# Performance work log

Measured on AMD Instinct MI355X. Metric: run time of the kernel, lower is better.

Reference implementation:

```python
import jax, jax.numpy as jnp
import numpy as np
from jax import lax

PEAK_THRESH = 0.1
PAF_SCORE_THRESH = 0.05
PAF_COUNT_THRESH = 0.8
P = 30   # max peaks kept per joint (vectorized stand-in for data-dependent nonzero())
S = 10   # samples along each limb line (torch.linspace steps=10)

# standard COCO person skeleton: 19 limbs over 17 keypoints
SKELETON = np.array([
    [15, 13], [13, 11], [16, 14], [14, 12], [11, 12], [5, 11], [6, 12], [5, 6],
    [5, 7], [6, 8], [7, 9], [8, 10], [1, 2], [0, 1], [0, 2], [1, 3], [2, 4],
    [3, 5], [4, 6],
])  # (L=19, 2)


def setup_inputs() -> dict:
    key = jax.random.key(0)
    k1, k2 = jax.random.split(key)
    heat_pred = jax.random.uniform(k1, (32, 17, 160, 160), dtype=jnp.float32)
    paf_pred = jax.random.normal(k2, (32, 38, 160, 160), dtype=jnp.float32)
    return {"heat_pred": heat_pred, "paf_pred": paf_pred}


def _forward(heat_pred, paf_pred):
    B, K, H, W = heat_pred.shape
    L = SKELETON.shape[0]

    # ---- 3x3 peak NMS (max_pool2d k=3, s=1, p=1) ----
    pooled = lax.reduce_window(heat_pred, -jnp.inf, lax.max,
                               (1, 1, 3, 3), (1, 1, 1, 1), 'SAME')
    is_peak = (heat_pred == pooled) & (heat_pred > PEAK_THRESH)

    # ---- dense subpixel (1D Newton) offsets ----
    r = jnp.roll(heat_pred, -1, -1); l = jnp.roll(heat_pred, 1, -1)
    d = jnp.roll(heat_pred, -1, -2); u = jnp.roll(heat_pred, 1, -2)
    dx_raw = 0.5 * (r - l); dy_raw = 0.5 * (d - u)
    dxx = r + l - 2.0 * heat_pred; dyy = d + u - 2.0 * heat_pred
    safe_dxx = jnp.where(jnp.abs(dxx) > 1e-6, -dxx, 1.0)
    safe_dyy = jnp.where(jnp.abs(dyy) > 1e-6, -dyy, 1.0)
    dx = jnp.where(jnp.abs(dxx) > 1e-6, dx_raw / safe_dxx, dx_raw)
    dy = jnp.where(jnp.abs(dyy) > 1e-6, dy_raw / safe_dyy, dy_raw)
    xi = jnp.arange(W); yi = jnp.arange(H)
    interior = (((yi > 0) & (yi < H - 1))[:, None]
                & ((xi > 0) & (xi < W - 1))[None, :])
    dx = jnp.where(interior, dx, 0.0)
    dy = jnp.where(interior, dy, 0.0)

    # ---- top-P peaks per (batch, joint) ----
    NEG = jnp.float32(-1e9)
    flat = jnp.where(is_peak, heat_pred, NEG).reshape(B, K, H * W)
    scores, idx = lax.top_k(flat, P)                    # (B, K, P)
    valid = scores > PEAK_THRESH
    py = (idx // W).astype(jnp.float32)
    px = (idx % W).astype(jnp.float32)
    dxp = jnp.take_along_axis(dx.reshape(B, K, H * W), idx, axis=2)
    dyp = jnp.take_along_axis(dy.reshape(B, K, H * W), idx, axis=2)
    px = jnp.where(valid, px + dxp, 0.0)
    py = jnp.where(valid, py + dyp, 0.0)
    sc = jnp.where(valid, scores, 0.0)
    peaks = jnp.stack([px, py, sc], axis=-1)            # (B, K, P, 3)

    # ---- PAF line-integral connection scores for all candidate pairs ----
    a = SKELETON[:, 0]; b = SKELETON[:, 1]
    ax, ay, sa, va = px[:, a], py[:, a], sc[:, a], valid[:, a]   # (B, L, P)
    bx, by, sb, vb = px[:, b], py[:, b], sc[:, b], valid[:, b]
    dxl = bx[:, :, None, :] - ax[:, :, :, None]          # (B, L, P, P)
    dyl = by[:, :, None, :] - ay[:, :, :, None]
    norm = jnp.sqrt(dxl * dxl + dyl * dyl) + 1e-8
    vx = dxl / norm; vy = dyl / norm
    t = jnp.linspace(0.0, 1.0, S, dtype=jnp.float32)     # (S,)
    xs = ax[:, :, :, None, None] + t * dxl[..., None]    # (B, L, P, P, S)
    ys = ay[:, :, :, None, None] + t * dyl[..., None]
    ix = jnp.clip(jnp.round(xs), 0, W - 1).astype(jnp.int32)
    iy = jnp.clip(jnp.round(ys), 0, H - 1).astype(jnp.int32)
    lin = (iy * W + ix).reshape(B, L, P * P * S)
    paf = paf_pred.reshape(B, L, 2, H * W)
    vals_x = jnp.take_along_axis(paf[:, :, 0], lin, axis=2).reshape(B, L, P, P, S)
    vals_y = jnp.take_along_axis(paf[:, :, 1], lin, axis=2).reshape(B, L, P, P, S)
    vecs = vals_x * vx[..., None] + vals_y * vy[..., None]
    mean_score = vecs.mean(-1)                            # (B, L, P, P)
    valid_ratio = (vecs > PAF_SCORE_THRESH).astype(jnp.float32).mean(-1)
    pair_valid = va[:, :, :, None] & vb[:, :, None, :]
    cond = (mean_score > 0.0) & (valid_ratio > PAF_COUNT_THRESH) & pair_valid
    conn = jnp.where(cond,
                     mean_score + 0.5 * (sa[:, :, :, None] + sb[:, :, None, :]),
                     0.0)                                 # (B, L, P, P)
    return peaks, conn


def reference(heat_pred, paf_pred):
    return _forward(heat_pred, paf_pred)
```

## Files before the change

### kernel.cpp

```cpp
#include <hip/hip_runtime.h>
#include <cstdint>
#include <cstddef>
#include <cfloat>

static constexpr int BATCH = 32;
static constexpr int KJ    = 17;
static constexpr int LL    = 19;
static constexpr int HH    = 160;
static constexpr int WW    = 160;
static constexpr int PPK   = 30;
static constexpr int SS    = 10;
static constexpr int HW    = HH * WW;
static constexpr int CGW   = WW / 4;
static constexpr int CAP   = 4096;
static constexpr int HICAP = 512;
static constexpr int NPAIR = PPK * PPK;
static constexpr int HALFP = NPAIR / 2;
#define HITHR 0.98f

static constexpr int QROWS = 40;
static constexpr int QCNT  = QROWS * WW;
static constexpr int QF4   = QCNT / 4;

__constant__ int d_ska[LL] = {15,13,16,14,11,5,6,5,5,6,7,8,1,0,0,1,2,3,4};
__constant__ int d_skb[LL] = {13,11,14,12,12,11,12,6,7,8,9,10,2,1,2,3,4,5,6};
__constant__ float d_ts[SS] = {
    0.0f,
    (float)(1.0/9.0), (float)(2.0/9.0), (float)(3.0/9.0),
    (float)(4.0/9.0), (float)(5.0/9.0), (float)(6.0/9.0),
    (float)(7.0/9.0), (float)(8.0/9.0),
    1.0f
};

__device__ __forceinline__ float max3f(float a, float b, float c) {
    return fmaxf(fmaxf(a, b), c);
}
__device__ __forceinline__ unsigned long long umax64(unsigned long long a, unsigned long long b) {
    return a > b ? a : b;
}
__device__ __forceinline__ void async_copy16(const float4* gsrc_lane, float4* lds_wave_base) {
    __builtin_amdgcn_global_load_lds(
        (const __attribute__((address_space(1))) void*)gsrc_lane,
        (__attribute__((address_space(3))) void*)lds_wave_base,
        16, 0, 0);
}

__global__ __launch_bounds__(512, 4) void peaks_kernel(const float* __restrict__ heat,
                                                       float* __restrict__ out)
{
    const int ch = blockIdx.x;
    const float* hp = heat + (size_t)ch * HW;

    __shared__ unsigned long long keys[CAP];
    __shared__ unsigned long long hikeys[HICAP];
    __shared__ unsigned long long sel8[8 * PPK];
    __shared__ unsigned long long sel[PPK];
    __shared__ int cnt;
    __shared__ int hcnt;

    const int tid  = threadIdx.x;
    const int lane = tid & 63;
    const int wave = tid >> 6;
    const unsigned long long ltmask = ((unsigned long long)1 << lane) - 1ull;

    if (tid == 0) { cnt = 0; hcnt = 0; }
    __syncthreads();

    for (int c = tid; c < HW / 4; c += 512) {
        int y  = c / CGW;
        int cg = c - y * CGW;
        int x0 = cg * 4;
        int yu = (y > 0) ? y - 1 : 0;
        int yd = (y < HH - 1) ? y + 1 : HH - 1;

        const float* rc = hp + y  * WW + x0;
        const float* ru = hp + yu * WW + x0;
        const float* rd = hp + yd * WW + x0;

        float4 vc = *(const float4*)rc;
        float4 vu = *(const float4*)ru;
        float4 vd = *(const float4*)rd;

        int offL = (x0 > 0) ? -1 : 0;
        int offR = (x0 + 4 < WW) ? 4 : 3;
        float lc  = rc[offL], lu  = ru[offL], ld  = rd[offL];
        float rcx = rc[offR], rux = ru[offR], rdx = rd[offR];

        float mu0 = max3f(lu, vu.x, vu.y), mu1 = max3f(vu.x, vu.y, vu.z);
        float mu2 = max3f(vu.y, vu.z, vu.w), mu3 = max3f(vu.z, vu.w, rux);
        float mc0 = max3f(lc, vc.x, vc.y), mc1 = max3f(vc.x, vc.y, vc.z);
        float mc2 = max3f(vc.y, vc.z, vc.w), mc3 = max3f(vc.z, vc.w, rcx);
        float md0 = max3f(ld, vd.x, vd.y), md1 = max3f(vd.x, vd.y, vd.z);
        float md2 = max3f(vd.y, vd.z, vd.w), md3 = max3f(vd.z, vd.w, rdx);

        float nm0 = max3f(mu0, mc0, md0);
        float nm1 = max3f(mu1, mc1, md1);
        float nm2 = max3f(mu2, mc2, md2);
        float nm3 = max3f(mu3, mc3, md3);

        bool pk0 = (vc.x == nm0) && (vc.x > 0.1f);
        bool pk1 = (vc.y == nm1) && (vc.y > 0.1f);
        bool pk2 = (vc.z == nm2) && (vc.z > 0.1f);
        bool pk3 = (vc.w == nm3) && (vc.w > 0.1f);

        int idx0 = y * WW + x0;
        unsigned long long key0 = ((unsigned long long)__float_as_uint(vc.x) << 32) | (unsigned long long)(0xFFFFFFFFu - (unsigned)(idx0 + 0));
        unsigned long long key1 = ((unsigned long long)__float_as_uint(vc.y) << 32) | (unsigned long long)(0xFFFFFFFFu - (unsigned)(idx0 + 1));
        unsigned long long key2 = ((unsigned long long)__float_as_uint(vc.z) << 32) | (unsigned long long)(0xFFFFFFFFu - (unsigned)(idx0 + 2));
        unsigned long long key3 = ((unsigned long long)__float_as_uint(vc.w) << 32) | (unsigned long long)(0xFFFFFFFFu - (unsigned)(idx0 + 3));

        {
            unsigned long long b0 = __ballot(pk0);
            unsigned long long b1 = __ballot(pk1);
            unsigned long long b2 = __ballot(pk2);
            unsigned long long b3 = __ballot(pk3);
            int c0 = __popcll(b0), c1 = __popcll(b1), c2 = __popcll(b2), c3 = __popcll(b3);
            int tot = c0 + c1 + c2 + c3;
            int base = 0;
            if (lane == 0 && tot > 0) base = atomicAdd(&cnt, tot);
            base = __shfl(base, 0);
            if (pk0) { int s = base + __popcll(b0 & ltmask); if (s < CAP) keys[s] = key0; }
            if (pk1) { int s = base + c0 + __popcll(b1 & ltmask); if (s < CAP) keys[s] = key1; }
            if (pk2) { int s = base + c0 + c1 + __popcll(b2 & ltmask); if (s < CAP) keys[s] = key2; }
            if (pk3) { int s = base + c0 + c1 + c2 + __popcll(b3 & ltmask); if (s < CAP) keys[s] = key3; }
        }
        {
            bool h0 = pk0 && (vc.x > HITHR);
            bool h1 = pk1 && (vc.y > HITHR);
            bool h2 = pk2 && (vc.z > HITHR);
            bool h3 = pk3 && (vc.w > HITHR);
            unsigned long long b0 = __ballot(h0);
            unsigned long long b1 = __ballot(h1);
            unsigned long long b2 = __ballot(h2);
            unsigned long long b3 = __ballot(h3);
            int c0 = __popcll(b0), c1 = __popcll(b1), c2 = __popcll(b2), c3 = __popcll(b3);
            int tot = c0 + c1 + c2 + c3;
            int base = 0;
            if (lane == 0 && tot > 0) base = atomicAdd(&hcnt, tot);
            base = __shfl(base, 0);
            if (h0) { int s = base + __popcll(b0 & ltmask); if (s < HICAP) hikeys[s] = key0; }
            if (h1) { int s = base + c0 + __popcll(b1 & ltmask); if (s < HICAP) hikeys[s] = key1; }
            if (h2) { int s = base + c0 + c1 + __popcll(b2 & ltmask); if (s < HICAP) hikeys[s] = key2; }
            if (h3) { int s = base + c0 + c1 + c2 + __popcll(b3 & ltmask); if (s < HICAP) hikeys[s] = key3; }
        }
    }
    __syncthreads();

    const int hn = hcnt;
    if (hn >= PPK && hn <= HICAP) {
        if (wave == 0) {
            unsigned long long k[8];
            #pragma unroll
            for (int i = 0; i < 8; ++i) {
                int p = lane + i * 64;
                k[i] = (p < hn) ? hikeys[p] : 0ull;
            }
            for (int r = 0; r < PPK; ++r) {
                unsigned long long best = 0ull;
                #pragma unroll
                for (int i = 0; i < 8; ++i) best = umax64(best, k[i]);
                #pragma unroll
                for (int off = 1; off < 64; off <<= 1)
                    best = umax64(best, (unsigned long long)__shfl_xor((long long)best, off));
                if (best != 0ull) {
                    #pragma unroll
                    for (int i = 0; i < 8; ++i)
                        if (k[i] == best) k[i] = 0ull;
                }
                if (lane == 0) sel[r] = best;
            }
        }
    } else {
        const int n = (cnt < CAP) ? cnt : CAP;
        unsigned long long k[8];
        {
            int base0 = wave * 512 + lane;
            #pragma unroll
            for (int i = 0; i < 8; ++i) {
                int p = base0 + i * 64;
                k[i] = (p < n) ? keys[p] : 0ull;
            }
        }
        for (int r = 0; r < PPK; ++r) {
            unsigned long long best = 0ull;
            #pragma unroll
            for (int i = 0; i < 8; ++i) best = umax64(best, k[i]);
            #pragma unroll
            for (int off = 1; off < 64; off <<= 1)
                best = umax64(best, (unsigned long long)__shfl_xor((long long)best, off));
            if (best != 0ull) {
                #pragma unroll
                for (int i = 0; i < 8; ++i)
                    if (k[i] == best) k[i] = 0ull;
            }
            if (lane == 0) sel8[wave * PPK + r] = best;
        }
        __syncthreads();
        if (wave == 0) {
            unsigned long long m[4];
            #pragma unroll
            for (int i = 0; i < 4; ++i) {
                int p = lane + i * 64;
                m[i] = (p < 8 * PPK) ? sel8[p] : 0ull;
            }
            for (int r = 0; r < PPK; ++r) {
                unsigned long long best = umax64(umax64(m[0], m[1]), umax64(m[2], m[3]));
                #pragma unroll
                for (int off = 1; off < 64; off <<= 1)
                    best = umax64(best, (unsigned long long)__shfl_xor((long long)best, off));
                if (best != 0ull) {
                    #pragma unroll
                    for (int i = 0; i < 4; ++i)
                        if (m[i] == best) m[i] = 0ull;
                }
                if (lane == 0) sel[r] = best;
            }
        }
    }
    __syncthreads();

    if (tid < PPK) {
        unsigned long long g = sel[tid];
        float px = 0.0f, py = 0.0f, sc = 0.0f;
        if (g != 0ull) {
            float v = __uint_as_float((unsigned int)(g >> 32));
            int idx = (int)(0xFFFFFFFFu - (unsigned int)(g & 0xFFFFFFFFull));
            int y = idx / WW;
            int x = idx - y * WW;
            float dx = 0.0f, dy = 0.0f;
            if (x > 0 && x < WW - 1 && y > 0 && y < HH - 1) {
                float r_ = hp[y * WW + x + 1];
                float l_ = hp[y * WW + x - 1];
                float dn = hp[(y + 1) * WW + x];
                float up = hp[(y - 1) * WW + x];
                float dx_raw = 0.5f * (r_ - l_);
                float dy_raw = 0.5f * (dn - up);
                float dxx = __fsub_rn(__fadd_rn(r_, l_), 2.0f * v);
                float dyy = __fsub_rn(__fadd_rn(dn, up), 2.0f * v);
                dx = (fabsf(dxx) > 1e-6f) ? (dx_raw / (-dxx)) : dx_raw;
                dy = (fabsf(dyy) > 1e-6f) ? (dy_raw / (-dyy)) : dy_raw;
            }
            px = __fadd_rn((float)x, dx);
            py = __fadd_rn((float)y, dy);
            sc = v;
        }
        float* o = out + ((size_t)ch * PPK + tid) * 3;
        o[0] = px;
        o[1] = py;
        o[2] = sc;
    }
}

__global__ __launch_bounds__(512, 4) void conn_kernel(const float* __restrict__ paf,
                                                      const float* __restrict__ peaks,
                                                      float* __restrict__ conn)
{
    const int bl = blockIdx.x;
    const int b  = bl / LL;
    const int l  = bl - b * LL;

    __shared__ float buf[2][QCNT];
    __shared__ float As[PPK * 3];
    __shared__ float Bs[PPK * 3];

    const int tid  = threadIdx.x;
    const int lane = tid & 63;
    const int wave = tid >> 6;
    {
        const float* pa = peaks + (((size_t)b * KJ) + d_ska[l]) * (PPK * 3);
        const float* pb = peaks + (((size_t)b * KJ) + d_skb[l]) * (PPK * 3);
        if (tid < PPK * 3)            As[tid] = pa[tid];
        else if (tid < 2 * PPK * 3)   Bs[tid - PPK * 3] = pb[tid - PPK * 3];
    }

    const float*  src  = paf + (((size_t)b * (2 * LL)) + 2 * l) * HW;
    const float4* src4 = (const float4*)src;

    {
        float4* b4 = (float4*)buf[0];
        #pragma unroll
        for (int c = 0; c < 3; ++c)
            async_copy16(src4 + c * 512 + tid, b4 + c * 512 + wave * 64);
        if (wave == 0)
            async_copy16(src4 + 1536 + lane, b4 + 1536);
    }
    __syncthreads();

    const bool active = (tid < HALFP);
    const int p0 = active ? tid : (NPAIR - 1);
    const int p1 = active ? (tid + HALFP) : (NPAIR - 1);

    int   lin[2][SS];
    float accv[2][SS];
    float vxp[2], vyp[2], sap[2], sbp[2];

    #pragma unroll
    for (int q = 0; q < 2; ++q) {
        int p = (q == 0) ? p0 : p1;
        int i = p / PPK;
        int j = p - i * PPK;
        float ax = As[i * 3 + 0], ay = As[i * 3 + 1], sa = As[i * 3 + 2];
        float bx = Bs[j * 3 + 0], by = Bs[j * 3 + 1], sb = Bs[j * 3 + 2];
        float dxl = __fsub_rn(bx, ax);
        float dyl = __fsub_rn(by, ay);
        float nsq = __fadd_rn(__fmul_rn(dxl, dxl), __fmul_rn(dyl, dyl));
        float nrm = __fadd_rn(sqrtf(nsq), 1e-8f);
        vxp[q] = dxl / nrm;
        vyp[q] = dyl / nrm;
        sap[q] = sa;
        sbp[q] = sb;
        #pragma unroll
        for (int s = 0; s < SS; ++s) {
            float t  = d_ts[s];
            float xs = __fadd_rn(ax, __fmul_rn(t, dxl));
            float ys = __fadd_rn(ay, __fmul_rn(t, dyl));
            float rx = rintf(xs);
            float ry = rintf(ys);
            rx = fminf(fmaxf(rx, 0.0f), (float)(WW - 1));
            ry = fminf(fmaxf(ry, 0.0f), (float)(HH - 1));
            lin[q][s] = (int)ry * WW + (int)rx;
        }
    }

    for (int qq = 0; qq < 8; ++qq) {
        const int cur = qq & 1;
        if (qq < 7) {
            const int nq = qq + 1;
            const float4* s4 = (const float4*)(src + (size_t)(nq >> 2) * HW + (nq & 3) * QCNT);
            float4* b4 = (float4*)buf[1 - cur];
            #pragma unroll
            for (int c = 0; c < 3; ++c)
                async_copy16(s4 + c * 512 + tid, b4 + c * 512 + wave * 64);
            if (wave == 0)
                async_copy16(s4 + 1536 + lane, b4 + 1536);
        }
        const int comp = qq >> 2;
        const int lo   = (qq & 3) * QCNT;
        #pragma unroll
        for (int q = 0; q < 2; ++q) {
            #pragma unroll
            for (int s = 0; s < SS; ++s) {
                int lrel = lin[q][s] - lo;
                if ((unsigned)lrel < (unsigned)QCNT) {
                    float v = buf[cur][lrel];
                    if (comp == 0) accv[q][s] = __fmul_rn(v, vxp[q]);
                    else           accv[q][s] = __fadd_rn(accv[q][s], __fmul_rn(v, vyp[q]));
                }
            }
        }
        __syncthreads();
    }

    if (active) {
        #pragma unroll
        for (int q = 0; q < 2; ++q) {
            int p = (q == 0) ? p0 : p1;
            int cntc = 0;
            #pragma unroll
            for (int s = 0; s < SS; ++s)
                if (accv[q][s] > 0.05f) ++cntc;
            float s01 = __fadd_rn(accv[q][0], accv[q][1]);
            float s23 = __fadd_rn(accv[q][2], accv[q][3]);
            float s45 = __fadd_rn(accv[q][4], accv[q][5]);
            float s67 = __fadd_rn(accv[q][6], accv[q][7]);
            float sum = __fadd_rn(__fadd_rn(s01, s23), __fadd_rn(s45, s67));
            sum = __fadd_rn(sum, accv[q][8]);
            sum = __fadd_rn(sum, accv[q][9]);
            float mean = sum / 10.0f;
            bool va = sap[q] > 0.1f;
            bool vb = sbp[q] > 0.1f;
            bool cond = (mean > 0.0f) && (cntc >= 9) && va && vb;
            float val = 0.0f;
            if (cond) val = __fadd_rn(mean, __fmul_rn(0.5f, __fadd_rn(sap[q], sbp[q])));
            conn[(size_t)bl * NPAIR + p] = val;
        }
    }
}

extern "C" void kernel_launch(void* const* d_in, const int* in_sizes, int n_in,
                              void* d_out, int out_size, void* d_ws, size_t ws_size,
                              hipStream_t stream)
{
    const float* heat = (const float*)d_in[0];
    const float* paf  = (const float*)d_in[1];
    float* out = (float*)d_out;

    float* peaks_out = out;
    float* conn_out  = out + (size_t)BATCH * KJ * PPK * 3;

    hipLaunchKernelGGL(peaks_kernel, dim3(BATCH * KJ), dim3(512), 0, stream,
                       heat, peaks_out);
    hipLaunchKernelGGL(conn_kernel, dim3(BATCH * LL), dim3(512), 0, stream,
                       paf, peaks_out, conn_out);
}
```

Measured before the change: 289.4 us.

## Stage heatmap strips into LDS with double-buffered async copies in peaks kernel

Result: no change. 286.2 us (-1.1%).

```diff
diff --git a/kernel.cpp b/kernel.cpp
--- a/kernel.cpp
+++ b/kernel.cpp
@@ -11,12 +11,16 @@
 static constexpr int PPK   = 30;
 static constexpr int SS    = 10;
 static constexpr int HW    = HH * WW;
-static constexpr int CGW   = WW / 4;
-static constexpr int CAP   = 4096;
+static constexpr int CAP   = 3072;
 static constexpr int HICAP = 512;
 static constexpr int NPAIR = PPK * PPK;
 static constexpr int HALFP = NPAIR / 2;
 #define HITHR 0.98f
+
+static constexpr int NSTRIP = 10;
+static constexpr int SR     = 16;
+static constexpr int BROWS  = 18;
+static constexpr int BFLT   = BROWS * WW;
 
 static constexpr int QROWS = 40;
 static constexpr int QCNT  = QROWS * WW;
@@ -45,15 +49,16 @@
         16, 0, 0);
 }
 
-__global__ __launch_bounds__(512, 4) void peaks_kernel(const float* __restrict__ heat,
-                                                       float* __restrict__ out)
+__global__ __launch_bounds__(256) void peaks_kernel(const float* __restrict__ heat,
+                                                    float* __restrict__ out)
 {
     const int ch = blockIdx.x;
     const float* hp = heat + (size_t)ch * HW;
 
+    __shared__ float sbuf[2][BFLT];
     __shared__ unsigned long long keys[CAP];
     __shared__ unsigned long long hikeys[HICAP];
-    __shared__ unsigned long long sel8[8 * PPK];
+    __shared__ unsigned long long sel4[4 * PPK];
     __shared__ unsigned long long sel[PPK];
     __shared__ int cnt;
     __shared__ int hcnt;
@@ -64,87 +69,111 @@
     const unsigned long long ltmask = ((unsigned long long)1 << lane) - 1ull;
 
     if (tid == 0) { cnt = 0; hcnt = 0; }
+
+    auto dma_strip = [&](int s, int bb) {
+        int firstrow = (s == 0) ? 0 : s * SR - 1;
+        int lastrow  = (s == NSTRIP - 1) ? (HH - 1) : s * SR + SR;
+        int nf4      = (lastrow - firstrow + 1) * (WW / 4);
+        const float4* g  = (const float4*)(hp + firstrow * WW);
+        float4*       b4 = (float4*)sbuf[bb] + ((s == 0) ? (WW / 4) : 0);
+        for (int c = wave; c * 64 < nf4; c += 4) {
+            int idx = c * 64 + lane;
+            if (idx < nf4) async_copy16(g + idx, b4 + c * 64);
+        }
+    };
+
+    dma_strip(0, 0);
     __syncthreads();
 
-    for (int c = tid; c < HW / 4; c += 512) {
-        int y  = c / CGW;
-        int cg = c - y * CGW;
-        int x0 = cg * 4;
-        int yu = (y > 0) ? y - 1 : 0;
-        int yd = (y < HH - 1) ? y + 1 : HH - 1;
-
-        const float* rc = hp + y  * WW + x0;
-        const float* ru = hp + yu * WW + x0;
-        const float* rd = hp + yd * WW + x0;
-
-        float4 vc = *(const float4*)rc;
-        float4 vu = *(const float4*)ru;
-        float4 vd = *(const float4*)rd;
-
-        int offL = (x0 > 0) ? -1 : 0;
-        int offR = (x0 + 4 < WW) ? 4 : 3;
-        float lc  = rc[offL], lu  = ru[offL], ld  = rd[offL];
-        float rcx = rc[offR], rux = ru[offR], rdx = rd[offR];
-
-        float mu0 = max3f(lu, vu.x, vu.y), mu1 = max3f(vu.x, vu.y, vu.z);
-        float mu2 = max3f(vu.y, vu.z, vu.w), mu3 = max3f(vu.z, vu.w, rux);
-        float mc0 = max3f(lc, vc.x, vc.y), mc1 = max3f(vc.x, vc.y, vc.z);
-        float mc2 = max3f(vc.y, vc.z, vc.w), mc3 = max3f(vc.z, vc.w, rcx);
-        float md0 = max3f(ld, vd.x, vd.y), md1 = max3f(vd.x, vd.y, vd.z);
-        float md2 = max3f(vd.y, vd.z, vd.w), md3 = max3f(vd.z, vd.w, rdx);
-
-        float nm0 = max3f(mu0, mc0, md0);
-        float nm1 = max3f(mu1, mc1, md1);
-        float nm2 = max3f(mu2, mc2, md2);
-        float nm3 = max3f(mu3, mc3, md3);
-
-        bool pk0 = (vc.x == nm0) && (vc.x > 0.1f);
-        bool pk1 = (vc.y == nm1) && (vc.y > 0.1f);
-        bool pk2 = (vc.z == nm2) && (vc.z > 0.1f);
-        bool pk3 = (vc.w == nm3) && (vc.w > 0.1f);
-
-        int idx0 = y * WW + x0;
-        unsigned long long key0 = ((unsigned long long)__float_as_uint(vc.x) << 32) | (unsigned long long)(0xFFFFFFFFu - (unsigned)(idx0 + 0));
-        unsigned long long key1 = ((unsigned long long)__float_as_uint(vc.y) << 32) | (unsigned long long)(0xFFFFFFFFu - (unsigned)(idx0 + 1));
-        unsigned long long key2 = ((unsigned long long)__float_as_uint(vc.z) << 32) | (unsigned long long)(0xFFFFFFFFu - (unsigned)(idx0 + 2));
-        unsigned long long key3 = ((unsigned long long)__float_as_uint(vc.w) << 32) | (unsigned long long)(0xFFFFFFFFu - (unsigned)(idx0 + 3));
-
-        {
-            unsigned long long b0 = __ballot(pk0);
-            unsigned long long b1 = __ballot(pk1);
-            unsigned long long b2 = __ballot(pk2);
-            unsigned long long b3 = __ballot(pk3);
-            int c0 = __popcll(b0), c1 = __popcll(b1), c2 = __popcll(b2), c3 = __popcll(b3);
-            int tot = c0 + c1 + c2 + c3;
-            int base = 0;
-            if (lane == 0 && tot > 0) base = atomicAdd(&cnt, tot);
-            base = __shfl(base, 0);
-            if (pk0) { int s = base + __popcll(b0 & ltmask); if (s < CAP) keys[s] = key0; }
-            if (pk1) { int s = base + c0 + __popcll(b1 & ltmask); if (s < CAP) keys[s] = key1; }
-            if (pk2) { int s = base + c0 + c1 + __popcll(b2 & ltmask); if (s < CAP) keys[s] = key2; }
-            if (pk3) { int s = base + c0 + c1 + c2 + __popcll(b3 & ltmask); if (s < CAP) keys[s] = key3; }
-        }
-        {
-            bool h0 = pk0 && (vc.x > HITHR);
-            bool h1 = pk1 && (vc.y > HITHR);
-            bool h2 = pk2 && (vc.z > HITHR);
-            bool h3 = pk3 && (vc.w > HITHR);
-            unsigned long long b0 = __ballot(h0);
-            unsigned long long b1 = __ballot(h1);
-            unsigned long long b2 = __ballot(h2);
-            unsigned long long b3 = __ballot(h3);
-            int c0 = __popcll(b0), c1 = __popcll(b1), c2 = __popcll(b2), c3 = __popcll(b3);
-            int tot = c0 + c1 + c2 + c3;
-            int base = 0;
-            if (lane == 0 && tot > 0) base = atomicAdd(&hcnt, tot);
-            base = __shfl(base, 0);
-            if (h0) { int s = base + __popcll(b0 & ltmask); if (s < HICAP) hikeys[s] = key0; }
-            if (h1) { int s = base + c0 + __popcll(b1 & ltmask); if (s < HICAP) hikeys[s] = key1; }
-            if (h2) { int s = base + c0 + c1 + __popcll(b2 & ltmask); if (s < HICAP) hikeys[s] = key2; }
-            if (h3) { int s = base + c0 + c1 + c2 + __popcll(b3 & ltmask); if (s < HICAP) hikeys[s] = key3; }
-        }
-    }
-    __syncthreads();
+    for (int s = 0; s < NSTRIP; ++s) {
+        const int bb = s & 1;
+        if (s < NSTRIP - 1) dma_strip(s + 1, 1 - bb);
+
+        const float* sb   = sbuf[bb];
+        const int gbase   = s * SR - 1;
+        for (int cell = tid; cell < SR * (WW / 4); cell += 256) {
+            int ly = cell / (WW / 4);
+            int cg = cell - ly * (WW / 4);
+            int y  = s * SR + ly;
+            int x0 = cg * 4;
+            int lr = y - gbase;
+            int lu = ((y > 0) ? y - 1 : 0) - gbase;
+            int ld_ = ((y < HH - 1) ? y + 1 : HH - 1) - gbase;
+
+            const float* rc = sb + lr  * WW + x0;
+            const float* ru = sb + lu  * WW + x0;
+            const float* rd = sb + ld_ * WW + x0;
+
+            float4 vc = *(const float4*)rc;
+            float4 vu = *(const float4*)ru;
+            float4 vd = *(const float4*)rd;
+            int offL = (x0 > 0) ? -1 : 0;
+            int offR = (x0 + 4 < WW) ? 4 : 3;
+            float lc  = rc[offL], lu_ = ru[offL], ldd = rd[offL];
+            float rcx = rc[offR], rux = ru[offR], rdx = rd[offR];
+
+            float mu0 = max3f(lu_, vu.x, vu.y), mu1 = max3f(vu.x, vu.y, vu.z);
+            float mu2 = max3f(vu.y, vu.z, vu.w), mu3 = max3f(vu.z, vu.w, rux);
+            float mc0 = max3f(lc, vc.x, vc.y),  mc1 = max3f(vc.x, vc.y, vc.z);
+            float mc2 = max3f(vc.y, vc.z, vc.w), mc3 = max3f(vc.z, vc.w, rcx);
+            float md0 = max3f(ldd, vd.x, vd.y), md1 = max3f(vd.x, vd.y, vd.z);
+            float md2 = max3f(vd.y, vd.z, vd.w), md3 = max3f(vd.z, vd.w, rdx);
+
+            float nm0 = max3f(mu0, mc0, md0);
+            float nm1 = max3f(mu1, mc1, md1);
+            float nm2 = max3f(mu2, mc2, md2);
+            float nm3 = max3f(mu3, mc3, md3);
+
+            bool pk0 = (vc.x == nm0) && (vc.x > 0.1f);
+            bool pk1 = (vc.y == nm1) && (vc.y > 0.1f);
+            bool pk2 = (vc.z == nm2) && (vc.z > 0.1f);
+            bool pk3 = (vc.w == nm3) && (vc.w > 0.1f);
+
+            int idx0 = y * WW + x0;
+            unsigned long long key0 = ((unsigned long long)__float_as_uint(vc.x) << 32) | (unsigned long long)(0xFFFFFFFFu - (unsigned)(idx0 + 0));
+            unsigned long long key1 = ((unsigned long long)__float_as_uint(vc.y) << 32) | (unsigned long long)(0xFFFFFFFFu - (unsigned)(idx0 + 1));
+            unsigned long long key2 = ((unsigned long long)__float_as_uint(vc.z) << 32) | (unsigned long long)(0xFFFFFFFFu - (unsigned)(idx0 + 2));
+            unsigned long long key3 = ((unsigned long long)__float_as_uint(vc.w) << 32) | (unsigned long long)(0xFFFFFFFFu - (unsigned)(idx0 + 3));
+
+            {
+                unsigned long long b0 = __ballot(pk0);
+                unsigned long long b1 = __ballot(pk1);
+                unsigned long long b2 = __ballot(pk2);
+                unsigned long long b3 = __ballot(pk3);
+                int c0 = __popcll(b0), c1 = __popcll(b1), c2 = __popcll(b2), c3 = __popcll(b3);
+                int tot = c0 + c1 + c2 + c3;
+                int base = 0;
+                if (lane == 0 && tot > 0) base = atomicAdd(&cnt, tot);
+                base = __shfl(base, 0);
+                if (pk0) { int sl = base + __popcll(b0 & ltmask); if (sl < CAP) keys[sl] = key0; }
+                if (pk1) { int sl = base + c0 + __popcll(b1 & ltmask); if (sl < CAP) keys[sl] = key1; }
+                if (pk2) { int sl = base + c0 + c1 + __popcll(b2 & ltmask); if (sl < CAP) keys[sl] = key2; }
+                if (pk3) { int sl = base + c0 + c1 + c2 + __popcll(b3 & ltmask); if (sl < CAP) keys[sl] = key3; }
+            }
+            {
+                bool h0 = pk0 && (vc.x > HITHR);
+                bool h1 = pk1 && (vc.y > HITHR);
+                bool h2 = pk2 && (vc.z > HITHR);
+                bool h3 = pk3 && (vc.w > HITHR);
+                unsigned long long b0 = __ballot(h0);
+                unsigned long long b1 = __ballot(h1);
+                unsigned long long b2 = __ballot(h2);
+                unsigned long long b3 = __ballot(h3);
+                int c0 = __popcll(b0), c1 = __popcll(b1), c2 = __popcll(b2), c3 = __popcll(b3);
+                int tot = c0 + c1 + c2 + c3;
+                if (tot > 0) {
+                    int base = 0;
+                    if (lane == 0) base = atomicAdd(&hcnt, tot);
+                    base = __shfl(base, 0);
+                    if (h0) { int sl = base + __popcll(b0 & ltmask); if (sl < HICAP) hikeys[sl] = key0; }
+                    if (h1) { int sl = base + c0 + __popcll(b1 & ltmask); if (sl < HICAP) hikeys[sl] = key1; }
+                    if (h2) { int sl = base + c0 + c1 + __popcll(b2 & ltmask); if (sl < HICAP) hikeys[sl] = key2; }
+                    if (h3) { int sl = base + c0 + c1 + c2 + __popcll(b3 & ltmask); if (sl < HICAP) hikeys[sl] = key3; }
+                }
+            }
+        }
+        __syncthreads();
+    }
 
     const int hn = hcnt;
     if (hn >= PPK && hn <= HICAP) {
@@ -172,11 +201,11 @@
         }
     } else {
         const int n = (cnt < CAP) ? cnt : CAP;
-        unsigned long long k[8];
+        unsigned long long k[12];
         {
-            int base0 = wave * 512 + lane;
-            #pragma unroll
-            for (int i = 0; i < 8; ++i) {
+            int base0 = wave * 768 + lane;
+            #pragma unroll
+            for (int i = 0; i < 12; ++i) {
                 int p = base0 + i * 64;
                 k[i] = (p < n) ? keys[p] : 0ull;
             }
@@ -184,34 +213,29 @@
         for (int r = 0; r < PPK; ++r) {
             unsigned long long best = 0ull;
             #pragma unroll
-            for (int i = 0; i < 8; ++i) best = umax64(best, k[i]);
+            for (int i = 0; i < 12; ++i) best = umax64(best, k[i]);
             #pragma unroll
             for (int off = 1; off < 64; off <<= 1)
                 best = umax64(best, (unsigned long long)__shfl_xor((long long)best, off));
             if (best != 0ull) {
                 #pragma unroll
-                for (int i = 0; i < 8; ++i)
+                for (int i = 0; i < 12; ++i)
                     if (k[i] == best) k[i] = 0ull;
             }
-            if (lane == 0) sel8[wave * PPK + r] = best;
+            if (lane == 0) sel4[wave * PPK + r] = best;
         }
         __syncthreads();
         if (wave == 0) {
-            unsigned long long m[4];
-            #pragma unroll
-            for (int i = 0; i < 4; ++i) {
-                int p = lane + i * 64;
-                m[i] = (p < 8 * PPK) ? sel8[p] : 0ull;
-            }
+            unsigned long long m0 = (lane < 4 * PPK) ? sel4[lane] : 0ull;
+            unsigned long long m1 = (lane + 64 < 4 * PPK) ? sel4[lane + 64] : 0ull;
             for (int r = 0; r < PPK; ++r) {
-                unsigned long long best = umax64(umax64(m[0], m[1]), umax64(m[2], m[3]));
+                unsigned long long best = umax64(m0, m1);
                 #pragma unroll
                 for (int off = 1; off < 64; off <<= 1)
                     best = umax64(best, (unsigned long long)__shfl_xor((long long)best, off));
                 if (best != 0ull) {
-                    #pragma unroll
-                    for (int i = 0; i < 4; ++i)
-                        if (m[i] == best) m[i] = 0ull;
+                    if (m0 == best) m0 = 0ull;
+                    else if (m1 == best) m1 = 0ull;
                 }
                 if (lane == 0) sel[r] = best;
             }
@@ -388,7 +412,7 @@
     float* peaks_out = out;
     float* conn_out  = out + (size_t)BATCH * KJ * PPK * 3;
 
-    hipLaunchKernelGGL(peaks_kernel, dim3(BATCH * KJ), dim3(512), 0, stream,
+    hipLaunchKernelGGL(peaks_kernel, dim3(BATCH * KJ), dim3(256), 0, stream,
                        heat, peaks_out);
     hipLaunchKernelGGL(conn_kernel, dim3(BATCH * LL), dim3(512), 0, stream,
                        paf, peaks_out, conn_out);
```

## Split peak detection into strip-parallel high-threshold scan and selection kernels

Applied to the files above, without the earlier changes.

Measured after the change: 269.0 us. -7.0%, faster.

```diff
diff --git a/kernel.cpp b/kernel.cpp
--- a/kernel.cpp
+++ b/kernel.cpp
@@ -13,10 +13,17 @@
 static constexpr int HW    = HH * WW;
 static constexpr int CGW   = WW / 4;
 static constexpr int CAP   = 4096;
-static constexpr int HICAP = 512;
 static constexpr int NPAIR = PPK * PPK;
 static constexpr int HALFP = NPAIR / 2;
 #define HITHR 0.98f
+
+static constexpr int NSTR   = 4;
+static constexpr int SROWS  = HH / NSTR;
+static constexpr int SHICAP = 192;
+static constexpr int NCH    = BATCH * KJ;
+static constexpr size_t WS_KEYS_BYTES = (size_t)NCH * NSTR * SHICAP * 8;
+static constexpr size_t WS_CNT_BYTES  = (size_t)NCH * NSTR * 4;
+static constexpr size_t WS_NEED = WS_KEYS_BYTES + WS_CNT_BYTES;
 
 static constexpr int QROWS = 40;
 static constexpr int QCNT  = QROWS * WW;
@@ -45,14 +52,285 @@
         16, 0, 0);
 }
 
-__global__ __launch_bounds__(512, 4) void peaks_kernel(const float* __restrict__ heat,
+__global__ __launch_bounds__(256) void peaks_scan_hi(const float* __restrict__ heat,
+                                                     unsigned long long* __restrict__ wsk,
+                                                     int* __restrict__ wsc)
+{
+    const int blk   = blockIdx.x;
+    const int ch    = blk >> 2;
+    const int strip = blk & 3;
+    const int y0    = strip * SROWS;
+    const float* hp = heat + (size_t)ch * HW;
+
+    __shared__ unsigned long long hik[SHICAP];
+    __shared__ int hcnt;
+
+    const int tid  = threadIdx.x;
+    const int lane = tid & 63;
+    const unsigned long long ltmask = ((unsigned long long)1 << lane) - 1ull;
+
+    if (tid == 0) hcnt = 0;
+    __syncthreads();
+
+    for (int cell = tid; cell < SROWS * CGW; cell += 256) {
+        int ly = cell / CGW;
+        int cg = cell - ly * CGW;
+        int y  = y0 + ly;
+        int x0 = cg * 4;
+        const float* rc = hp + y * WW + x0;
+        float4 vc = *(const float4*)rc;
+
+        bool h_any = (vc.x > HITHR) || (vc.y > HITHR) || (vc.z > HITHR) || (vc.w > HITHR);
+        bool h0 = false, h1 = false, h2 = false, h3 = false;
+        if (__any(h_any ? 1 : 0)) {
+            int yu = (y > 0) ? y - 1 : 0;
+            int yd = (y < HH - 1) ? y + 1 : HH - 1;
+            const float* ru = hp + yu * WW + x0;
+            const float* rd = hp + yd * WW + x0;
+            float4 vu = *(const float4*)ru;
+            float4 vd = *(const float4*)rd;
+            int offL = (x0 > 0) ? -1 : 0;
+            int offR = (x0 + 4 < WW) ? 4 : 3;
+            float lc  = rc[offL], lu  = ru[offL], ld  = rd[offL];
+            float rcx = rc[offR], rux = ru[offR], rdx = rd[offR];
+
+            float mu0 = max3f(lu, vu.x, vu.y), mu1 = max3f(vu.x, vu.y, vu.z);
+            float mu2 = max3f(vu.y, vu.z, vu.w), mu3 = max3f(vu.z, vu.w, rux);
+            float mc0 = max3f(lc, vc.x, vc.y), mc1 = max3f(vc.x, vc.y, vc.z);
+            float mc2 = max3f(vc.y, vc.z, vc.w), mc3 = max3f(vc.z, vc.w, rcx);
+            float md0 = max3f(ld, vd.x, vd.y), md1 = max3f(vd.x, vd.y, vd.z);
+            float md2 = max3f(vd.y, vd.z, vd.w), md3 = max3f(vd.z, vd.w, rdx);
+
+            float nm0 = max3f(mu0, mc0, md0);
+            float nm1 = max3f(mu1, mc1, md1);
+            float nm2 = max3f(mu2, mc2, md2);
+            float nm3 = max3f(mu3, mc3, md3);
+
+            h0 = (vc.x == nm0) && (vc.x > HITHR);
+            h1 = (vc.y == nm1) && (vc.y > HITHR);
+            h2 = (vc.z == nm2) && (vc.z > HITHR);
+            h3 = (vc.w == nm3) && (vc.w > HITHR);
+        }
+        unsigned long long b0 = __ballot(h0);
+        unsigned long long b1 = __ballot(h1);
+        unsigned long long b2 = __ballot(h2);
+        unsigned long long b3 = __ballot(h3);
+        int c0 = __popcll(b0), c1 = __popcll(b1), c2 = __popcll(b2), c3 = __popcll(b3);
+        int tot = c0 + c1 + c2 + c3;
+        if (tot == 0) continue;
+        int base = 0;
+        if (lane == 0) base = atomicAdd(&hcnt, tot);
+        base = __shfl(base, 0);
+
+        int idx0 = y * WW + x0;
+        if (h0) { int s = base + __popcll(b0 & ltmask); if (s < SHICAP)
+            hik[s] = ((unsigned long long)__float_as_uint(vc.x) << 32) | (unsigned long long)(0xFFFFFFFFu - (unsigned)(idx0 + 0)); }
+        if (h1) { int s = base + c0 + __popcll(b1 & ltmask); if (s < SHICAP)
+            hik[s] = ((unsigned long long)__float_as_uint(vc.y) << 32) | (unsigned long long)(0xFFFFFFFFu - (unsigned)(idx0 + 1)); }
+        if (h2) { int s = base + c0 + c1 + __popcll(b2 & ltmask); if (s < SHICAP)
+            hik[s] = ((unsigned long long)__float_as_uint(vc.z) << 32) | (unsigned long long)(0xFFFFFFFFu - (unsigned)(idx0 + 2)); }
+        if (h3) { int s = base + c0 + c1 + c2 + __popcll(b3 & ltmask); if (s < SHICAP)
+            hik[s] = ((unsigned long long)__float_as_uint(vc.w) << 32) | (unsigned long long)(0xFFFFFFFFu - (unsigned)(idx0 + 3)); }
+    }
+    __syncthreads();
+
+    if (tid == 0) wsc[blk] = hcnt;
+    const int n = (hcnt < SHICAP) ? hcnt : SHICAP;
+    for (int i = tid; i < n; i += 256)
+        wsk[(size_t)blk * SHICAP + i] = hik[i];
+}
+
+__global__ __launch_bounds__(256, 4) void peaks_select(const float* __restrict__ heat,
+                                                       const unsigned long long* __restrict__ wsk,
+                                                       const int* __restrict__ wsc,
                                                        float* __restrict__ out)
 {
     const int ch = blockIdx.x;
     const float* hp = heat + (size_t)ch * HW;
 
     __shared__ unsigned long long keys[CAP];
-    __shared__ unsigned long long hikeys[HICAP];
+    __shared__ unsigned long long sel4[4 * PPK];
+    __shared__ unsigned long long sel[PPK];
+    __shared__ int cnt;
+
+    const int tid  = threadIdx.x;
+    const int lane = tid & 63;
+    const int wave = tid >> 6;
+    const unsigned long long ltmask = ((unsigned long long)1 << lane) - 1ull;
+
+    const int c0 = wsc[ch * 4 + 0];
+    const int c1 = wsc[ch * 4 + 1];
+    const int c2 = wsc[ch * 4 + 2];
+    const int c3 = wsc[ch * 4 + 3];
+    const bool ok = (c0 <= SHICAP) && (c1 <= SHICAP) && (c2 <= SHICAP) && (c3 <= SHICAP);
+    const int n = c0 + c1 + c2 + c3;
+
+    if (tid == 0) cnt = 0;
+
+    if (ok && n >= PPK) {
+        const int off1 = c0, off2 = c0 + c1, off3 = c0 + c1 + c2;
+        for (int i = tid; i < c0; i += 256) keys[i]        = wsk[(size_t)(ch * 4 + 0) * SHICAP + i];
+        for (int i = tid; i < c1; i += 256) keys[off1 + i] = wsk[(size_t)(ch * 4 + 1) * SHICAP + i];
+        for (int i = tid; i < c2; i += 256) keys[off2 + i] = wsk[(size_t)(ch * 4 + 2) * SHICAP + i];
+        for (int i = tid; i < c3; i += 256) keys[off3 + i] = wsk[(size_t)(ch * 4 + 3) * SHICAP + i];
+        __syncthreads();
+
+        unsigned long long mine0 = (tid < n)       ? keys[tid]       : 0ull;
+        unsigned long long mine1 = (tid + 256 < n) ? keys[tid + 256] : 0ull;
+        unsigned long long mine2 = (tid + 512 < n) ? keys[tid + 512] : 0ull;
+        int r0 = 0, r1 = 0, r2 = 0;
+        for (int j = 0; j < n; ++j) {
+            unsigned long long kj = keys[j];
+            r0 += (kj > mine0) ? 1 : 0;
+            r1 += (kj > mine1) ? 1 : 0;
+            r2 += (kj > mine2) ? 1 : 0;
+        }
+        if (tid < n       && r0 < PPK) sel[r0] = mine0;
+        if (tid + 256 < n && r1 < PPK) sel[r1] = mine1;
+        if (tid + 512 < n && r2 < PPK) sel[r2] = mine2;
+        __syncthreads();
+    } else {
+        __syncthreads();
+        for (int c = tid; c < HW / 4; c += 256) {
+            int y  = c / CGW;
+            int cg = c - y * CGW;
+            int x0 = cg * 4;
+            int yu = (y > 0) ? y - 1 : 0;
+            int yd = (y < HH - 1) ? y + 1 : HH - 1;
+            const float* rc = hp + y  * WW + x0;
+            const float* ru = hp + yu * WW + x0;
+            const float* rd = hp + yd * WW + x0;
+            float4 vc = *(const float4*)rc;
+            float4 vu = *(const float4*)ru;
+            float4 vd = *(const float4*)rd;
+            int offL = (x0 > 0) ? -1 : 0;
+            int offR = (x0 + 4 < WW) ? 4 : 3;
+            float lc  = rc[offL], lu  = ru[offL], ld  = rd[offL];
+            float rcx = rc[offR], rux = ru[offR], rdx = rd[offR];
+
+            float mu0 = max3f(lu, vu.x, vu.y), mu1 = max3f(vu.x, vu.y, vu.z);
+            float mu2 = max3f(vu.y, vu.z, vu.w), mu3 = max3f(vu.z, vu.w, rux);
+            float mc0 = max3f(lc, vc.x, vc.y), mc1 = max3f(vc.x, vc.y, vc.z);
+            float mc2 = max3f(vc.y, vc.z, vc.w), mc3 = max3f(vc.z, vc.w, rcx);
+            float md0 = max3f(ld, vd.x, vd.y), md1 = max3f(vd.x, vd.y, vd.z);
+            float md2 = max3f(vd.y, vd.z, vd.w), md3 = max3f(vd.z, vd.w, rdx);
+
+            float nm0 = max3f(mu0, mc0, md0);
+            float nm1 = max3f(mu1, mc1, md1);
+            float nm2 = max3f(mu2, mc2, md2);
+            float nm3 = max3f(mu3, mc3, md3);
+
+            bool pk0 = (vc.x == nm0) && (vc.x > 0.1f);
+            bool pk1 = (vc.y == nm1) && (vc.y > 0.1f);
+            bool pk2 = (vc.z == nm2) && (vc.z > 0.1f);
+            bool pk3 = (vc.w == nm3) && (vc.w > 0.1f);
+
+            unsigned long long b0 = __ballot(pk0);
+            unsigned long long b1 = __ballot(pk1);
+            unsigned long long b2 = __ballot(pk2);
+            unsigned long long b3 = __ballot(pk3);
+            int d0 = __popcll(b0), d1 = __popcll(b1), d2 = __popcll(b2), d3 = __popcll(b3);
+            int tot = d0 + d1 + d2 + d3;
+            int base = 0;
+            if (lane == 0 && tot > 0) base = atomicAdd(&cnt, tot);
+            base = __shfl(base, 0);
+
+            int idx0 = y * WW + x0;
+            if (pk0) { int s = base + __popcll(b0 & ltmask); if (s < CAP)
+                keys[s] = ((unsigned long long)__float_as_uint(vc.x) << 32) | (unsigned long long)(0xFFFFFFFFu - (unsigned)(idx0 + 0)); }
+            if (pk1) { int s = base + d0 + __popcll(b1 & ltmask); if (s < CAP)
+                keys[s] = ((unsigned long long)__float_as_uint(vc.y) << 32) | (unsigned long long)(0xFFFFFFFFu - (unsigned)(idx0 + 1)); }
+            if (pk2) { int s = base + d0 + d1 + __popcll(b2 & ltmask); if (s < CAP)
+                keys[s] = ((unsigned long long)__float_as_uint(vc.z) << 32) | (unsigned long long)(0xFFFFFFFFu - (unsigned)(idx0 + 2)); }
+            if (pk3) { int s = base + d0 + d1 + d2 + __popcll(b3 & ltmask); if (s < CAP)
+                keys[s] = ((unsigned long long)__float_as_uint(vc.w) << 32) | (unsigned long long)(0xFFFFFFFFu - (unsigned)(idx0 + 3)); }
+        }
+        __syncthreads();
+
+        const int m = (cnt < CAP) ? cnt : CAP;
+        unsigned long long k[16];
+        {
+            int base0 = wave * 1024 + lane;
+            #pragma unroll
+            for (int i = 0; i < 16; ++i) {
+                int p = base0 + i * 64;
+                k[i] = (p < m) ? keys[p] : 0ull;
+            }
+        }
+        for (int r = 0; r < PPK; ++r) {
+            unsigned long long best = 0ull;
+            #pragma unroll
+            for (int i = 0; i < 16; ++i) best = umax64(best, k[i]);
+            #pragma unroll
+            for (int off = 1; off < 64; off <<= 1)
+                best = umax64(best, (unsigned long long)__shfl_xor((long long)best, off));
+            if (best != 0ull) {
+                #pragma unroll
+                for (int i = 0; i < 16; ++i)
+                    if (k[i] == best) k[i] = 0ull;
+            }
+            if (lane == 0) sel4[wave * PPK + r] = best;
+        }
+        __syncthreads();
+        if (wave == 0) {
+            unsigned long long m0 = (lane < 4 * PPK) ? sel4[lane] : 0ull;
+            unsigned long long m1 = (lane + 64 < 4 * PPK) ? sel4[lane + 64] : 0ull;
+            for (int r = 0; r < PPK; ++r) {
+                unsigned long long best = umax64(m0, m1);
+                #pragma unroll
+                for (int off = 1; off < 64; off <<= 1)
+                    best = umax64(best, (unsigned long long)__shfl_xor((long long)best, off));
+                if (best != 0ull) {
+                    if (m0 == best) m0 = 0ull;
+                    else if (m1 == best) m1 = 0ull;
+                }
+                if (lane == 0) sel[r] = best;
+            }
+        }
+        __syncthreads();
+    }
+
+    if (tid < PPK) {
+        unsigned long long g = sel[tid];
+        float px = 0.0f, py = 0.0f, sc = 0.0f;
+        if (g != 0ull) {
+            float v = __uint_as_float((unsigned int)(g >> 32));
+            int idx = (int)(0xFFFFFFFFu - (unsigned int)(g & 0xFFFFFFFFull));
+            int y = idx / WW;
+            int x = idx - y * WW;
+            float dx = 0.0f, dy = 0.0f;
+            if (x > 0 && x < WW - 1 && y > 0 && y < HH - 1) {
+                float r_ = hp[y * WW + x + 1];
+                float l_ = hp[y * WW + x - 1];
+                float dn = hp[(y + 1) * WW + x];
+                float up = hp[(y - 1) * WW + x];
+                float dx_raw = 0.5f * (r_ - l_);
+                float dy_raw = 0.5f * (dn - up);
+                float dxx = __fsub_rn(__fadd_rn(r_, l_), 2.0f * v);
+                float dyy = __fsub_rn(__fadd_rn(dn, up), 2.0f * v);
+                dx = (fabsf(dxx) > 1e-6f) ? (dx_raw / (-dxx)) : dx_raw;
+                dy = (fabsf(dyy) > 1e-6f) ? (dy_raw / (-dyy)) : dy_raw;
+            }
+            px = __fadd_rn((float)x, dx);
+            py = __fadd_rn((float)y, dy);
+            sc = v;
+        }
+        float* o = out + ((size_t)ch * PPK + tid) * 3;
+        o[0] = px;
+        o[1] = py;
+        o[2] = sc;
+    }
+}
+
+static constexpr int FHICAP = 512;
+__global__ __launch_bounds__(512, 4) void peaks_fused(const float* __restrict__ heat,
+                                                      float* __restrict__ out)
+{
+    const int ch = blockIdx.x;
+    const float* hp = heat + (size_t)ch * HW;
+
+    __shared__ unsigned long long keys[CAP];
+    __shared__ unsigned long long hikeys[FHICAP];
     __shared__ unsigned long long sel8[8 * PPK];
     __shared__ unsigned long long sel[PPK];
     __shared__ int cnt;
@@ -72,43 +350,35 @@
         int x0 = cg * 4;
         int yu = (y > 0) ? y - 1 : 0;
         int yd = (y < HH - 1) ? y + 1 : HH - 1;
-
         const float* rc = hp + y  * WW + x0;
         const float* ru = hp + yu * WW + x0;
         const float* rd = hp + yd * WW + x0;
-
         float4 vc = *(const float4*)rc;
         float4 vu = *(const float4*)ru;
         float4 vd = *(const float4*)rd;
-
         int offL = (x0 > 0) ? -1 : 0;
         int offR = (x0 + 4 < WW) ? 4 : 3;
         float lc  = rc[offL], lu  = ru[offL], ld  = rd[offL];
         float rcx = rc[offR], rux = ru[offR], rdx = rd[offR];
-
         float mu0 = max3f(lu, vu.x, vu.y), mu1 = max3f(vu.x, vu.y, vu.z);
         float mu2 = max3f(vu.y, vu.z, vu.w), mu3 = max3f(vu.z, vu.w, rux);
         float mc0 = max3f(lc, vc.x, vc.y), mc1 = max3f(vc.x, vc.y, vc.z);
         float mc2 = max3f(vc.y, vc.z, vc.w), mc3 = max3f(vc.z, vc.w, rcx);
         float md0 = max3f(ld, vd.x, vd.y), md1 = max3f(vd.x, vd.y, vd.z);
         float md2 = max3f(vd.y, vd.z, vd.w), md3 = max3f(vd.z, vd.w, rdx);
-
         float nm0 = max3f(mu0, mc0, md0);
         float nm1 = max3f(mu1, mc1, md1);
         float nm2 = max3f(mu2, mc2, md2);
         float nm3 = max3f(mu3, mc3, md3);
-
         bool pk0 = (vc.x == nm0) && (vc.x > 0.1f);
         bool pk1 = (vc.y == nm1) && (vc.y > 0.1f);
         bool pk2 = (vc.z == nm2) && (vc.z > 0.1f);
         bool pk3 = (vc.w == nm3) && (vc.w > 0.1f);
-
         int idx0 = y * WW + x0;
         unsigned long long key0 = ((unsigned long long)__float_as_uint(vc.x) << 32) | (unsigned long long)(0xFFFFFFFFu - (unsigned)(idx0 + 0));
         unsigned long long key1 = ((unsigned long long)__float_as_uint(vc.y) << 32) | (unsigned long long)(0xFFFFFFFFu - (unsigned)(idx0 + 1));
         unsigned long long key2 = ((unsigned long long)__float_as_uint(vc.z) << 32) | (unsigned long long)(0xFFFFFFFFu - (unsigned)(idx0 + 2));
         unsigned long long key3 = ((unsigned long long)__float_as_uint(vc.w) << 32) | (unsigned long long)(0xFFFFFFFFu - (unsigned)(idx0 + 3));
-
         {
             unsigned long long b0 = __ballot(pk0);
             unsigned long long b1 = __ballot(pk1);
@@ -135,19 +405,21 @@
             unsigned long long b3 = __ballot(h3);
             int c0 = __popcll(b0), c1 = __popcll(b1), c2 = __popcll(b2), c3 = __popcll(b3);
             int tot = c0 + c1 + c2 + c3;
-            int base = 0;
-            if (lane == 0 && tot > 0) base = atomicAdd(&hcnt, tot);
-            base = __shfl(base, 0);
-            if (h0) { int s = base + __popcll(b0 & ltmask); if (s < HICAP) hikeys[s] = key0; }
-            if (h1) { int s = base + c0 + __popcll(b1 & ltmask); if (s < HICAP) hikeys[s] = key1; }
-            if (h2) { int s = base + c0 + c1 + __popcll(b2 & ltmask); if (s < HICAP) hikeys[s] = key2; }
-            if (h3) { int s = base + c0 + c1 + c2 + __popcll(b3 & ltmask); if (s < HICAP) hikeys[s] = key3; }
+            if (tot > 0) {
+                int base = 0;
+                if (lane == 0) base = atomicAdd(&hcnt, tot);
+                base = __shfl(base, 0);
+                if (h0) { int s = base + __popcll(b0 & ltmask); if (s < FHICAP) hikeys[s] = key0; }
+                if (h1) { int s = base + c0 + __popcll(b1 & ltmask); if (s < FHICAP) hikeys[s] = key1; }
+                if (h2) { int s = base + c0 + c1 + __popcll(b2 & ltmask); if (s < FHICAP) hikeys[s] = key2; }
+                if (h3) { int s = base + c0 + c1 + c2 + __popcll(b3 & ltmask); if (s < FHICAP) hikeys[s] = key3; }
+            }
         }
     }
     __syncthreads();
 
     const int hn = hcnt;
-    if (hn >= PPK && hn <= HICAP) {
+    if (hn >= PPK && hn <= FHICAP) {
         if (wave == 0) {
             unsigned long long k[8];
             #pragma unroll
@@ -388,8 +660,17 @@
     float* peaks_out = out;
     float* conn_out  = out + (size_t)BATCH * KJ * PPK * 3;
 
-    hipLaunchKernelGGL(peaks_kernel, dim3(BATCH * KJ), dim3(512), 0, stream,
-                       heat, peaks_out);
+    if (ws_size >= WS_NEED) {
+        unsigned long long* wsk = (unsigned long long*)d_ws;
+        int* wsc = (int*)((char*)d_ws + WS_KEYS_BYTES);
+        hipLaunchKernelGGL(peaks_scan_hi, dim3(NCH * NSTR), dim3(256), 0, stream,
+                           heat, wsk, wsc);
+        hipLaunchKernelGGL(peaks_select, dim3(NCH), dim3(256), 0, stream,
+                           heat, wsk, wsc, peaks_out);
+    } else {
+        hipLaunchKernelGGL(peaks_fused, dim3(NCH), dim3(512), 0, stream,
+                           heat, peaks_out);
+    }
     hipLaunchKernelGGL(conn_kernel, dim3(BATCH * LL), dim3(512), 0, stream,
                        paf, peaks_out, conn_out);
 }
```
